# Performance work log

Hardware: AMD Instinct MI355X
Metric: run time of the kernel (lower is better)

## Reference

```python
import jax, jax.numpy as jnp
import numpy as np

DIM = 192
HEADS = 6
WS = 7
N = WS * WS  # 49
B_ = 4096
NW = 64


def _relative_position_index(ws):
    coords = np.stack(np.meshgrid(np.arange(ws), np.arange(ws), indexing='ij'))  # (2, ws, ws)
    cf = coords.reshape(2, -1)  # (2, N)
    rel = cf[:, :, None] - cf[:, None, :]  # (2, N, N)
    rel = rel.transpose(1, 2, 0).copy()
    rel[:, :, 0] += ws - 1
    rel[:, :, 1] += ws - 1
    rel[:, :, 0] *= 2 * ws - 1
    return jnp.asarray(rel.sum(-1), dtype=jnp.int32)  # (N, N)


def setup_inputs() -> dict:
    key = jax.random.key(0)
    ks = jax.random.split(key, 8)
    x = jax.random.normal(ks[0], (B_, N, DIM), dtype=jnp.float32)
    mask = jax.random.normal(ks[1], (NW, N, N), dtype=jnp.float32)
    qkv_w = jax.random.normal(ks[2], (3 * DIM, DIM), dtype=jnp.float32) * 0.02
    qkv_b = jnp.zeros((3 * DIM,), dtype=jnp.float32)
    proj_w = jax.random.normal(ks[3], (DIM, DIM), dtype=jnp.float32) * 0.02
    proj_b = jnp.zeros((DIM,), dtype=jnp.float32)
    n_bias = (2 * WS - 1) * (2 * WS - 1)  # 169
    bias_table = jax.random.truncated_normal(ks[4], -2.0, 2.0, (n_bias, HEADS), dtype=jnp.float32) * 0.02
    rel_idx = _relative_position_index(WS)
    return {"x": x, "mask": mask, "qkv_w": qkv_w, "qkv_b": qkv_b,
            "proj_w": proj_w, "proj_b": proj_b, "bias_table": bias_table,
            "rel_idx": rel_idx}


def reference(x, mask, qkv_w, qkv_b, proj_w, proj_b, bias_table, rel_idx):
    Bw, n, c = x.shape
    hd = c // HEADS
    scale = hd ** -0.5
    qkv = x @ qkv_w.T + qkv_b  # (B_, N, 3C)
    qkv = qkv.reshape(Bw, n, 3, HEADS, hd).transpose(2, 0, 3, 1, 4)  # (3, B_, H, N, hd)
    q, k, v = qkv[0] * scale, qkv[1], qkv[2]
    attn = jnp.einsum('bhqd,bhkd->bhqk', q, k)  # (B_, H, N, N)
    bias = bias_table[rel_idx.reshape(-1)].reshape(n, n, HEADS).transpose(2, 0, 1)  # (H, N, N)
    attn = attn + bias[None]
    nW = mask.shape[0]
    attn = attn.reshape(Bw // nW, nW, HEADS, n, n) + mask[None, :, None]
    attn = jax.nn.softmax(attn.reshape(Bw, HEADS, n, n), axis=-1)
    out = jnp.einsum('bhqk,bhkd->bhqd', attn, v)  # (B_, H, N, hd)
    out = out.transpose(0, 2, 1, 3).reshape(Bw, n, c)
    return out @ proj_w.T + proj_b
```

## Files before the change

### kernel.cpp

```cpp
#include <hip/hip_runtime.h>
#include <hip/hip_fp16.h>


typedef short bf16x8 __attribute__((ext_vector_type(8)));
typedef float f32x4 __attribute__((ext_vector_type(4)));

#define MFMA16(a, b, c) __builtin_amdgcn_mfma_f32_16x16x32_bf16((a), (b), (c), 0, 0, 0)

#define DIMC 192
#define NTOK 49

__device__ __forceinline__ unsigned short f2bf(float f) {
  unsigned int u = __float_as_uint(f);
  u += 0x7fffu + ((u >> 16) & 1u);
  return (unsigned short)(u >> 16);
}

__device__ __forceinline__ unsigned int cvt_pk_bf16(float lo, float hi) {
  unsigned int r;
  asm("v_cvt_pk_bf16_f32 %0, %1, %2" : "=v"(r) : "v"(lo), "v"(hi));
  return r;
}

__global__ void prep_kernel(const float* __restrict__ qkv_w,
                            const float* __restrict__ proj_w,
                            const float* __restrict__ bias_table,
                            const int* __restrict__ rel_idx,
                            const float* __restrict__ mask,
                            unsigned short* __restrict__ qkv_wb,
                            unsigned short* __restrict__ proj_wb,
                            __half* __restrict__ bmT) {
  int i = blockIdx.x * 256 + threadIdx.x;
  if (i < 576 * 192) qkv_wb[i] = f2bf(qkv_w[i]);
  if (i < 192 * 192) proj_wb[i] = f2bf(proj_w[i]);
  {
    int r = i & 3;
    int q = (i >> 2) & 63;
    int lq = (i >> 8) & 3;
    int nt = (i >> 10) & 3;
    int hw = i >> 12;
    int h = hw % 6;
    int widx = hw / 6;
    int k = nt * 16 + lq * 4 + r;
    float v;
    if (k >= NTOK) v = -30000.f;
    else if (q >= NTOK) v = 0.f;
    else v = bias_table[rel_idx[q * NTOK + k] * 6 + h] +
             mask[(size_t)widx * (NTOK * NTOK) + q * NTOK + k];
    bmT[i] = __float2half(v);
  }
}

__global__ __launch_bounds__(256, 4) void winattn_kernel(
    const float* __restrict__ x,
    const float* __restrict__ qkv_b,
    const float* __restrict__ proj_b,
    const unsigned short* __restrict__ qkv_wb,
    const unsigned short* __restrict__ proj_wb,
    const __half* __restrict__ bmT,
    float* __restrict__ out) {
  __shared__ unsigned short xb[64 * 200];
  __shared__ unsigned short Qs[64 * 40];
  __shared__ unsigned short Ks[64 * 40];
  __shared__ unsigned short Vts[32 * 72];

  const int tid = threadIdx.x;
  const int b = blockIdx.x;
  const int widx = b & 63;
  const int lane = tid & 63;
  const int wv = tid >> 6;
  const int lq = lane >> 4;
  const int ln = lane & 15;

  {
    const float4* xp = (const float4*)(x + (size_t)b * (NTOK * DIMC));
    for (int i = tid; i < NTOK * DIMC / 4; i += 256) {
      float4 v = xp[i];
      int fl = i * 4;
      int r = fl / DIMC;
      int c = fl - r * DIMC;
      unsigned int lo = (unsigned int)f2bf(v.x) | ((unsigned int)f2bf(v.y) << 16);
      unsigned int hi = (unsigned int)f2bf(v.z) | ((unsigned int)f2bf(v.w) << 16);
      *(uint2*)(&xb[r * 200 + c]) = make_uint2(lo, hi);
    }
    for (int i = tid; i < 15 * 200 / 2; i += 256)
      ((unsigned int*)(&xb[49 * 200]))[i] = 0u;
  }

  f32x4 pacc[12];
#pragma unroll
  for (int nti = 0; nti < 12; ++nti) {
    float pbv = proj_b[nti * 16 + ln];
    pacc[nti] = (f32x4){pbv, pbv, pbv, pbv};
  }
  __syncthreads();

  const float scale = 0.17677669529663687f;
  const __half* bmp = bmT + (size_t)widx * 6 * 4096;
  const int sA = ((lq & 1) << 5) | ln;
  const int sB = sA + 16;
  const int hiSel = lq >> 1;

  for (int h = 0; h < 6; ++h) {
    uint2 bmu[4];
    {
      const __half* bmh = bmp + (size_t)h * 4096;
#pragma unroll
      for (int nt = 0; nt < 4; ++nt)
        bmu[nt] = *(const uint2*)(bmh + ((nt * 4 + lq) * 64 + wv * 16 + ln) * 4);
    }

    for (int tt = 0; tt < 6; tt += 2) {
      int t0 = wv * 6 + tt;
      int t1 = t0 + 1;
      int nt0 = t0 >> 2, mt0 = t0 & 3;
      int nt1 = t1 >> 2, mt1 = t1 & 3;
      int oc0 = (nt0 >> 1) * DIMC + h * 32 + (nt0 & 1) * 16 + ln;
      int oc1 = (nt1 >> 1) * DIMC + h * 32 + (nt1 & 1) * 16 + ln;
      const unsigned short* w0p = qkv_wb + (size_t)oc0 * DIMC + lq * 8;
      const unsigned short* w1p = qkv_wb + (size_t)oc1 * DIMC + lq * 8;
      bf16x8 w0[6], w1[6];
#pragma unroll
      for (int ks = 0; ks < 6; ++ks) {
        w0[ks] = *(const bf16x8*)(w0p + ks * 32);
        w1[ks] = *(const bf16x8*)(w1p + ks * 32);
      }
      float b0 = qkv_b[oc0], b1 = qkv_b[oc1];
      f32x4 acc0 = (f32x4){b0, b0, b0, b0};
      f32x4 acc1 = (f32x4){b1, b1, b1, b1};
      const unsigned short* a0p = &xb[(mt0 * 16 + ln) * 200 + lq * 8];
      const unsigned short* a1p = &xb[(mt1 * 16 + ln) * 200 + lq * 8];
#pragma unroll
      for (int ks = 0; ks < 6; ++ks) {
        bf16x8 a0 = *(const bf16x8*)(a0p + ks * 32);
        bf16x8 a1 = *(const bf16x8*)(a1p + ks * 32);
        acc0 = MFMA16(a0, w0[ks], acc0);
        acc1 = MFMA16(a1, w1[ks], acc1);
      }
      {
        int which = nt0 >> 1, db = (nt0 & 1) * 16 + ln, row0 = mt0 * 16 + lq * 4;
        if (which == 0) {
#pragma unroll
          for (int r = 0; r < 4; ++r) Qs[(row0 + r) * 40 + db] = f2bf(acc0[r] * scale);
        } else if (which == 1) {
#pragma unroll
          for (int r = 0; r < 4; ++r) Ks[(row0 + r) * 40 + db] = f2bf(acc0[r]);
        } else {
          unsigned int lo = cvt_pk_bf16(acc0[0], acc0[1]);
          unsigned int hi = cvt_pk_bf16(acc0[2], acc0[3]);
          *(uint2*)(&Vts[db * 72 + row0]) = make_uint2(lo, hi);
        }
      }
      {
        int which = nt1 >> 1, db = (nt1 & 1) * 16 + ln, row0 = mt1 * 16 + lq * 4;
        if (which == 0) {
#pragma unroll
          for (int r = 0; r < 4; ++r) Qs[(row0 + r) * 40 + db] = f2bf(acc1[r] * scale);
        } else if (which == 1) {
#pragma unroll
          for (int r = 0; r < 4; ++r) Ks[(row0 + r) * 40 + db] = f2bf(acc1[r]);
        } else {
          unsigned int lo = cvt_pk_bf16(acc1[0], acc1[1]);
          unsigned int hi = cvt_pk_bf16(acc1[2], acc1[3]);
          *(uint2*)(&Vts[db * 72 + row0]) = make_uint2(lo, hi);
        }
      }
    }
    __syncthreads();

    {
      bf16x8 qf = *(const bf16x8*)&Qs[(wv * 16 + ln) * 40 + lq * 8];
      f32x4 sv[4];
#pragma unroll
      for (int nt = 0; nt < 4; ++nt) {
        bf16x8 kf = *(const bf16x8*)&Ks[(nt * 16 + ln) * 40 + lq * 8];
        sv[nt] = MFMA16(kf, qf, ((f32x4){0.f, 0.f, 0.f, 0.f}));
      }
      float tt[4][4];
#pragma unroll
      for (int nt = 0; nt < 4; ++nt) {
        float2 f01 = __half22float2(*(const __half2*)&bmu[nt].x);
        float2 f23 = __half22float2(*(const __half2*)&bmu[nt].y);
        tt[nt][0] = sv[nt][0] + f01.x;
        tt[nt][1] = sv[nt][1] + f01.y;
        tt[nt][2] = sv[nt][2] + f23.x;
        tt[nt][3] = sv[nt][3] + f23.y;
      }
      float m = tt[0][0];
#pragma unroll
      for (int nt = 0; nt < 4; ++nt)
#pragma unroll
        for (int r = 0; r < 4; ++r) m = fmaxf(m, tt[nt][r]);
      m = fmaxf(m, __shfl_xor(m, 16, 64));
      m = fmaxf(m, __shfl_xor(m, 32, 64));
      float sum = 0.f;
#pragma unroll
      for (int nt = 0; nt < 4; ++nt)
#pragma unroll
        for (int r = 0; r < 4; ++r) {
          float e = __expf(tt[nt][r] - m);
          tt[nt][r] = e;
          sum += e;
        }
      sum += __shfl_xor(sum, 16, 64);
      sum += __shfl_xor(sum, 32, 64);
      float pinv = 1.f / sum;

      unsigned int pk[4][2];
#pragma unroll
      for (int nt = 0; nt < 4; ++nt) {
        pk[nt][0] = cvt_pk_bf16(tt[nt][0], tt[nt][1]);
        pk[nt][1] = cvt_pk_bf16(tt[nt][2], tt[nt][3]);
      }
      union U8 { unsigned int u[4]; bf16x8 v; };
      U8 pb0, pb1;
#pragma unroll
      for (int w = 0; w < 4; ++w) {
        int src = (w & 2) ? sB : sA;
        int a0 = __shfl((int)pk[0][w & 1], src, 64);
        int a1 = __shfl((int)pk[1][w & 1], src, 64);
        int b0 = __shfl((int)pk[2][w & 1], src, 64);
        int b1 = __shfl((int)pk[3][w & 1], src, 64);
        pb0.u[w] = (unsigned int)(hiSel ? a1 : a0);
        pb1.u[w] = (unsigned int)(hiSel ? b1 : b0);
      }
      f32x4 o[2];
#pragma unroll
      for (int db = 0; db < 2; ++db) {
        bf16x8 v0 = *(const bf16x8*)&Vts[(db * 16 + ln) * 72 + lq * 8];
        bf16x8 v1 = *(const bf16x8*)&Vts[(db * 16 + ln) * 72 + 32 + lq * 8];
        f32x4 acc = (f32x4){0.f, 0.f, 0.f, 0.f};
        acc = MFMA16(v0, pb0.v, acc);
        acc = MFMA16(v1, pb1.v, acc);
        o[db] = acc;
      }
      unsigned int pkO[2][2];
#pragma unroll
      for (int db = 0; db < 2; ++db) {
        pkO[db][0] = cvt_pk_bf16(o[db][0] * pinv, o[db][1] * pinv);
        pkO[db][1] = cvt_pk_bf16(o[db][2] * pinv, o[db][3] * pinv);
      }
      U8 oa;
#pragma unroll
      for (int w = 0; w < 4; ++w) {
        int src = (w & 2) ? sB : sA;
        int a0 = __shfl((int)pkO[0][w & 1], src, 64);
        int a1 = __shfl((int)pkO[1][w & 1], src, 64);
        oa.u[w] = (unsigned int)(hiSel ? a1 : a0);
      }
#pragma unroll
      for (int nti = 0; nti < 12; ++nti) {
        bf16x8 w = *(const bf16x8*)(proj_wb + (size_t)(nti * 16 + ln) * DIMC + h * 32 + lq * 8);
        pacc[nti] = MFMA16(oa.v, w, pacc[nti]);
      }
    }
    __syncthreads();
  }

  {
    float* outp = out + (size_t)b * (NTOK * DIMC);
#pragma unroll
    for (int nti = 0; nti < 12; ++nti) {
      int col = nti * 16 + ln;
#pragma unroll
      for (int r = 0; r < 4; ++r) {
        int row = wv * 16 + lq * 4 + r;
        if (row < NTOK) outp[row * DIMC + col] = pacc[nti][r];
      }
    }
  }
}

extern "C" void kernel_launch(void* const* d_in, const int* in_sizes, int n_in,
                              void* d_out, int out_size, void* d_ws, size_t ws_size,
                              hipStream_t stream) {
  const float* x = (const float*)d_in[0];
  const float* mask = (const float*)d_in[1];
  const float* qkv_w = (const float*)d_in[2];
  const float* qkv_b = (const float*)d_in[3];
  const float* proj_w = (const float*)d_in[4];
  const float* proj_b = (const float*)d_in[5];
  const float* bias_table = (const float*)d_in[6];
  const int* rel_idx = (const int*)d_in[7];

  unsigned short* qkv_wb = (unsigned short*)d_ws;
  unsigned short* proj_wb = qkv_wb + 576 * 192;
  __half* bmT = (__half*)(proj_wb + 192 * 192);

  prep_kernel<<<6144, 256, 0, stream>>>(qkv_w, proj_w, bias_table, rel_idx,
                                        mask, qkv_wb, proj_wb, bmT);
  winattn_kernel<<<4096, 256, 0, stream>>>(x, qkv_b, proj_b,
                                           qkv_wb, proj_wb, bmT,
                                           (float*)d_out);
}
```

Measured before the change: 627.5 us.

## Compute full QKV projection upfront with register-cached x fragments

Instead of computing Q/K/V per head inside the head loop, each wave loads all x fragments into registers once and computes the full 576-column QKV projection before the attention loop. Results go into a shared pool that aliases the x buffer, and the per-head loop then needs no barriers. Launch bounds drop from 4 to 2 blocks per CU to make room for the 96 extra fragment registers and the larger shared footprint (~77KB), which lowers occupancy.

New measurement: 528.3 us. 15.8% less time.

```diff
diff --git a/kernel.cpp b/kernel.cpp
--- a/kernel.cpp
+++ b/kernel.cpp
@@ -51,7 +51,7 @@
   }
 }
 
-__global__ __launch_bounds__(256, 4) void winattn_kernel(
+__global__ __launch_bounds__(256, 2) void winattn_kernel(
     const float* __restrict__ x,
     const float* __restrict__ qkv_b,
     const float* __restrict__ proj_b,
@@ -59,10 +59,11 @@
     const unsigned short* __restrict__ proj_wb,
     const __half* __restrict__ bmT,
     float* __restrict__ out) {
-  __shared__ unsigned short xb[64 * 200];
-  __shared__ unsigned short Qs[64 * 40];
-  __shared__ unsigned short Ks[64 * 40];
-  __shared__ unsigned short Vts[32 * 72];
+  __shared__ unsigned short pool[39424];
+  unsigned short* xb   = pool;
+  unsigned short* Qall = pool;
+  unsigned short* Kall = pool + 12800;
+  unsigned short* Vta  = pool + 25600;
 
   const int tid = threadIdx.x;
   const int b = blockIdx.x;
@@ -86,6 +87,65 @@
     for (int i = tid; i < 15 * 200 / 2; i += 256)
       ((unsigned int*)(&xb[49 * 200]))[i] = 0u;
   }
+  __syncthreads();
+
+  bf16x8 af[4][6];
+#pragma unroll
+  for (int mt = 0; mt < 4; ++mt)
+#pragma unroll
+    for (int ks = 0; ks < 6; ++ks)
+      af[mt][ks] = *(const bf16x8*)&xb[(mt * 16 + ln) * 200 + ks * 32 + lq * 8];
+  __syncthreads();
+
+  const float scale = 0.17677669529663687f;
+
+  for (int i = 0; i < 9; ++i) {
+    int nt = wv * 9 + i;
+    int c = nt * 16 + ln;
+    const unsigned short* wp = qkv_wb + (size_t)c * DIMC + lq * 8;
+    bf16x8 wf[6];
+#pragma unroll
+    for (int ks = 0; ks < 6; ++ks) wf[ks] = *(const bf16x8*)(wp + ks * 32);
+    float bv = qkv_b[c];
+    f32x4 a0 = (f32x4){bv, bv, bv, bv};
+    f32x4 a1 = a0, a2 = a0, a3 = a0;
+#pragma unroll
+    for (int ks = 0; ks < 6; ++ks) {
+      a0 = MFMA16(af[0][ks], wf[ks], a0);
+      a1 = MFMA16(af[1][ks], wf[ks], a1);
+      a2 = MFMA16(af[2][ks], wf[ks], a2);
+      a3 = MFMA16(af[3][ks], wf[ks], a3);
+    }
+    f32x4 acc[4] = {a0, a1, a2, a3};
+    int which = nt / 12;
+    int colq = c - which * 192;
+    if (which == 0) {
+#pragma unroll
+      for (int mt = 0; mt < 4; ++mt) {
+        int row0 = mt * 16 + lq * 4;
+#pragma unroll
+        for (int r = 0; r < 4; ++r)
+          Qall[(row0 + r) * 200 + colq] = f2bf(acc[mt][r] * scale);
+      }
+    } else if (which == 1) {
+#pragma unroll
+      for (int mt = 0; mt < 4; ++mt) {
+        int row0 = mt * 16 + lq * 4;
+#pragma unroll
+        for (int r = 0; r < 4; ++r)
+          Kall[(row0 + r) * 200 + colq] = f2bf(acc[mt][r]);
+      }
+    } else {
+#pragma unroll
+      for (int mt = 0; mt < 4; ++mt) {
+        int row0 = mt * 16 + lq * 4;
+        unsigned int lo = cvt_pk_bf16(acc[mt][0], acc[mt][1]);
+        unsigned int hi = cvt_pk_bf16(acc[mt][2], acc[mt][3]);
+        *(uint2*)(&Vta[colq * 72 + row0]) = make_uint2(lo, hi);
+      }
+    }
+  }
+  __syncthreads();
 
   f32x4 pacc[12];
 #pragma unroll
@@ -93,9 +153,7 @@
     float pbv = proj_b[nti * 16 + ln];
     pacc[nti] = (f32x4){pbv, pbv, pbv, pbv};
   }
-  __syncthreads();
-
-  const float scale = 0.17677669529663687f;
+
   const __half* bmp = bmT + (size_t)widx * 6 * 4096;
   const int sA = ((lq & 1) << 5) | ln;
   const int sB = sA + 16;
@@ -110,151 +168,90 @@
         bmu[nt] = *(const uint2*)(bmh + ((nt * 4 + lq) * 64 + wv * 16 + ln) * 4);
     }
 
-    for (int tt = 0; tt < 6; tt += 2) {
-      int t0 = wv * 6 + tt;
-      int t1 = t0 + 1;
-      int nt0 = t0 >> 2, mt0 = t0 & 3;
-      int nt1 = t1 >> 2, mt1 = t1 & 3;
-      int oc0 = (nt0 >> 1) * DIMC + h * 32 + (nt0 & 1) * 16 + ln;
-      int oc1 = (nt1 >> 1) * DIMC + h * 32 + (nt1 & 1) * 16 + ln;
-      const unsigned short* w0p = qkv_wb + (size_t)oc0 * DIMC + lq * 8;
-      const unsigned short* w1p = qkv_wb + (size_t)oc1 * DIMC + lq * 8;
-      bf16x8 w0[6], w1[6];
-#pragma unroll
-      for (int ks = 0; ks < 6; ++ks) {
-        w0[ks] = *(const bf16x8*)(w0p + ks * 32);
-        w1[ks] = *(const bf16x8*)(w1p + ks * 32);
-      }
-      float b0 = qkv_b[oc0], b1 = qkv_b[oc1];
-      f32x4 acc0 = (f32x4){b0, b0, b0, b0};
-      f32x4 acc1 = (f32x4){b1, b1, b1, b1};
-      const unsigned short* a0p = &xb[(mt0 * 16 + ln) * 200 + lq * 8];
-      const unsigned short* a1p = &xb[(mt1 * 16 + ln) * 200 + lq * 8];
-#pragma unroll
-      for (int ks = 0; ks < 6; ++ks) {
-        bf16x8 a0 = *(const bf16x8*)(a0p + ks * 32);
-        bf16x8 a1 = *(const bf16x8*)(a1p + ks * 32);
-        acc0 = MFMA16(a0, w0[ks], acc0);
-        acc1 = MFMA16(a1, w1[ks], acc1);
-      }
-      {
-        int which = nt0 >> 1, db = (nt0 & 1) * 16 + ln, row0 = mt0 * 16 + lq * 4;
-        if (which == 0) {
-#pragma unroll
-          for (int r = 0; r < 4; ++r) Qs[(row0 + r) * 40 + db] = f2bf(acc0[r] * scale);
-        } else if (which == 1) {
-#pragma unroll
-          for (int r = 0; r < 4; ++r) Ks[(row0 + r) * 40 + db] = f2bf(acc0[r]);
-        } else {
-          unsigned int lo = cvt_pk_bf16(acc0[0], acc0[1]);
-          unsigned int hi = cvt_pk_bf16(acc0[2], acc0[3]);
-          *(uint2*)(&Vts[db * 72 + row0]) = make_uint2(lo, hi);
-        }
-      }
-      {
-        int which = nt1 >> 1, db = (nt1 & 1) * 16 + ln, row0 = mt1 * 16 + lq * 4;
-        if (which == 0) {
-#pragma unroll
-          for (int r = 0; r < 4; ++r) Qs[(row0 + r) * 40 + db] = f2bf(acc1[r] * scale);
-        } else if (which == 1) {
-#pragma unroll
-          for (int r = 0; r < 4; ++r) Ks[(row0 + r) * 40 + db] = f2bf(acc1[r]);
-        } else {
-          unsigned int lo = cvt_pk_bf16(acc1[0], acc1[1]);
-          unsigned int hi = cvt_pk_bf16(acc1[2], acc1[3]);
-          *(uint2*)(&Vts[db * 72 + row0]) = make_uint2(lo, hi);
-        }
-      }
-    }
-    __syncthreads();
-
-    {
-      bf16x8 qf = *(const bf16x8*)&Qs[(wv * 16 + ln) * 40 + lq * 8];
-      f32x4 sv[4];
-#pragma unroll
-      for (int nt = 0; nt < 4; ++nt) {
-        bf16x8 kf = *(const bf16x8*)&Ks[(nt * 16 + ln) * 40 + lq * 8];
-        sv[nt] = MFMA16(kf, qf, ((f32x4){0.f, 0.f, 0.f, 0.f}));
-      }
-      float tt[4][4];
-#pragma unroll
-      for (int nt = 0; nt < 4; ++nt) {
-        float2 f01 = __half22float2(*(const __half2*)&bmu[nt].x);
-        float2 f23 = __half22float2(*(const __half2*)&bmu[nt].y);
-        tt[nt][0] = sv[nt][0] + f01.x;
-        tt[nt][1] = sv[nt][1] + f01.y;
-        tt[nt][2] = sv[nt][2] + f23.x;
-        tt[nt][3] = sv[nt][3] + f23.y;
-      }
-      float m = tt[0][0];
-#pragma unroll
-      for (int nt = 0; nt < 4; ++nt)
-#pragma unroll
-        for (int r = 0; r < 4; ++r) m = fmaxf(m, tt[nt][r]);
-      m = fmaxf(m, __shfl_xor(m, 16, 64));
-      m = fmaxf(m, __shfl_xor(m, 32, 64));
-      float sum = 0.f;
-#pragma unroll
-      for (int nt = 0; nt < 4; ++nt)
-#pragma unroll
-        for (int r = 0; r < 4; ++r) {
-          float e = __expf(tt[nt][r] - m);
-          tt[nt][r] = e;
-          sum += e;
-        }
-      sum += __shfl_xor(sum, 16, 64);
-      sum += __shfl_xor(sum, 32, 64);
-      float pinv = 1.f / sum;
-
-      unsigned int pk[4][2];
-#pragma unroll
-      for (int nt = 0; nt < 4; ++nt) {
-        pk[nt][0] = cvt_pk_bf16(tt[nt][0], tt[nt][1]);
-        pk[nt][1] = cvt_pk_bf16(tt[nt][2], tt[nt][3]);
-      }
-      union U8 { unsigned int u[4]; bf16x8 v; };
-      U8 pb0, pb1;
-#pragma unroll
-      for (int w = 0; w < 4; ++w) {
-        int src = (w & 2) ? sB : sA;
-        int a0 = __shfl((int)pk[0][w & 1], src, 64);
-        int a1 = __shfl((int)pk[1][w & 1], src, 64);
-        int b0 = __shfl((int)pk[2][w & 1], src, 64);
-        int b1 = __shfl((int)pk[3][w & 1], src, 64);
-        pb0.u[w] = (unsigned int)(hiSel ? a1 : a0);
-        pb1.u[w] = (unsigned int)(hiSel ? b1 : b0);
-      }
-      f32x4 o[2];
-#pragma unroll
-      for (int db = 0; db < 2; ++db) {
-        bf16x8 v0 = *(const bf16x8*)&Vts[(db * 16 + ln) * 72 + lq * 8];
-        bf16x8 v1 = *(const bf16x8*)&Vts[(db * 16 + ln) * 72 + 32 + lq * 8];
-        f32x4 acc = (f32x4){0.f, 0.f, 0.f, 0.f};
-        acc = MFMA16(v0, pb0.v, acc);
-        acc = MFMA16(v1, pb1.v, acc);
-        o[db] = acc;
-      }
-      unsigned int pkO[2][2];
-#pragma unroll
-      for (int db = 0; db < 2; ++db) {
-        pkO[db][0] = cvt_pk_bf16(o[db][0] * pinv, o[db][1] * pinv);
-        pkO[db][1] = cvt_pk_bf16(o[db][2] * pinv, o[db][3] * pinv);
-      }
-      U8 oa;
-#pragma unroll
-      for (int w = 0; w < 4; ++w) {
-        int src = (w & 2) ? sB : sA;
-        int a0 = __shfl((int)pkO[0][w & 1], src, 64);
-        int a1 = __shfl((int)pkO[1][w & 1], src, 64);
-        oa.u[w] = (unsigned int)(hiSel ? a1 : a0);
-      }
-#pragma unroll
-      for (int nti = 0; nti < 12; ++nti) {
-        bf16x8 w = *(const bf16x8*)(proj_wb + (size_t)(nti * 16 + ln) * DIMC + h * 32 + lq * 8);
-        pacc[nti] = MFMA16(oa.v, w, pacc[nti]);
-      }
-    }
-    __syncthreads();
+    bf16x8 qf = *(const bf16x8*)&Qall[(wv * 16 + ln) * 200 + h * 32 + lq * 8];
+    f32x4 sv[4];
+#pragma unroll
+    for (int nt = 0; nt < 4; ++nt) {
+      bf16x8 kf = *(const bf16x8*)&Kall[(nt * 16 + ln) * 200 + h * 32 + lq * 8];
+      sv[nt] = MFMA16(kf, qf, ((f32x4){0.f, 0.f, 0.f, 0.f}));
+    }
+    float tt[4][4];
+#pragma unroll
+    for (int nt = 0; nt < 4; ++nt) {
+      float2 f01 = __half22float2(*(const __half2*)&bmu[nt].x);
+      float2 f23 = __half22float2(*(const __half2*)&bmu[nt].y);
+      tt[nt][0] = sv[nt][0] + f01.x;
+      tt[nt][1] = sv[nt][1] + f01.y;
+      tt[nt][2] = sv[nt][2] + f23.x;
+      tt[nt][3] = sv[nt][3] + f23.y;
+    }
+    float m = tt[0][0];
+#pragma unroll
+    for (int nt = 0; nt < 4; ++nt)
+#pragma unroll
+      for (int r = 0; r < 4; ++r) m = fmaxf(m, tt[nt][r]);
+    m = fmaxf(m, __shfl_xor(m, 16, 64));
+    m = fmaxf(m, __shfl_xor(m, 32, 64));
+    float sum = 0.f;
+#pragma unroll
+    for (int nt = 0; nt < 4; ++nt)
+#pragma unroll
+      for (int r = 0; r < 4; ++r) {
+        float e = __expf(tt[nt][r] - m);
+        tt[nt][r] = e;
+        sum += e;
+      }
+    sum += __shfl_xor(sum, 16, 64);
+    sum += __shfl_xor(sum, 32, 64);
+    float pinv = 1.f / sum;
+
+    unsigned int pk[4][2];
+#pragma unroll
+    for (int nt = 0; nt < 4; ++nt) {
+      pk[nt][0] = cvt_pk_bf16(tt[nt][0], tt[nt][1]);
+      pk[nt][1] = cvt_pk_bf16(tt[nt][2], tt[nt][3]);
+    }
+    union U8 { unsigned int u[4]; bf16x8 v; };
+    U8 pb0, pb1;
+#pragma unroll
+    for (int w = 0; w < 4; ++w) {
+      int src = (w & 2) ? sB : sA;
+      int a0 = __shfl((int)pk[0][w & 1], src, 64);
+      int a1 = __shfl((int)pk[1][w & 1], src, 64);
+      int b0 = __shfl((int)pk[2][w & 1], src, 64);
+      int b1 = __shfl((int)pk[3][w & 1], src, 64);
+      pb0.u[w] = (unsigned int)(hiSel ? a1 : a0);
+      pb1.u[w] = (unsigned int)(hiSel ? b1 : b0);
+    }
+    f32x4 o[2];
+#pragma unroll
+    for (int db = 0; db < 2; ++db) {
+      bf16x8 v0 = *(const bf16x8*)&Vta[(h * 32 + db * 16 + ln) * 72 + lq * 8];
+      bf16x8 v1 = *(const bf16x8*)&Vta[(h * 32 + db * 16 + ln) * 72 + 32 + lq * 8];
+      f32x4 acc = (f32x4){0.f, 0.f, 0.f, 0.f};
+      acc = MFMA16(v0, pb0.v, acc);
+      acc = MFMA16(v1, pb1.v, acc);
+      o[db] = acc;
+    }
+    unsigned int pkO[2][2];
+#pragma unroll
+    for (int db = 0; db < 2; ++db) {
+      pkO[db][0] = cvt_pk_bf16(o[db][0] * pinv, o[db][1] * pinv);
+      pkO[db][1] = cvt_pk_bf16(o[db][2] * pinv, o[db][3] * pinv);
+    }
+    U8 oa;
+#pragma unroll
+    for (int w = 0; w < 4; ++w) {
+      int src = (w & 2) ? sB : sA;
+      int a0 = __shfl((int)pkO[0][w & 1], src, 64);
+      int a1 = __shfl((int)pkO[1][w & 1], src, 64);
+      oa.u[w] = (unsigned int)(hiSel ? a1 : a0);
+    }
+#pragma unroll
+    for (int nti = 0; nti < 12; ++nti) {
+      bf16x8 w = *(const bf16x8*)(proj_wb + (size_t)(nti * 16 + ln) * DIMC + h * 32 + lq * 8);
+      pacc[nti] = MFMA16(oa.v, w, pacc[nti]);
+    }
   }
 
   {
```
